# Performance work log

Hardware: AMD Instinct MI355X
Metric: run time of the kernel (lower is better)

## Reference

```python
import jax, jax.numpy as jnp
import numpy as np

N = 50000          # nodes
E = 800000         # edges (avg degree 16)
D = 128            # feature dim
MSG_EPS = 1e-7     # GENConv eps added to relu(msg)
SM_EPS = 1e-16     # pyg softmax denominator eps
BN_EPS = 1e-5
LN_EPS = 1e-5


def setup_inputs() -> dict:
    key = jax.random.key(0)
    ks = jax.random.split(key, 6)
    x = jax.random.normal(ks[0], (N, D), dtype=jnp.float32)
    edge_index = jax.random.randint(ks[1], (2, E), 0, N, dtype=jnp.int32)
    t = jnp.array(1.0, dtype=jnp.float32)
    W1 = jax.random.normal(ks[2], (D, 2 * D), dtype=jnp.float32) / np.sqrt(D).astype(np.float32)
    b1 = jnp.zeros((2 * D,), jnp.float32)
    bn_gamma = jnp.ones((2 * D,), jnp.float32)
    bn_beta = jnp.zeros((2 * D,), jnp.float32)
    W2 = jax.random.normal(ks[3], (2 * D, D), dtype=jnp.float32) / np.sqrt(2 * D).astype(np.float32)
    b2 = jnp.zeros((D,), jnp.float32)
    ln_gamma = jnp.ones((D,), jnp.float32)
    ln_beta = jnp.zeros((D,), jnp.float32)
    return {"x": x, "edge_index": edge_index, "t": t, "W1": W1, "b1": b1,
            "bn_gamma": bn_gamma, "bn_beta": bn_beta, "W2": W2, "b2": b2,
            "ln_gamma": ln_gamma, "ln_beta": ln_beta}


def reference(x, edge_index, t, W1, b1, bn_gamma, bn_beta, W2, b2, ln_gamma, ln_beta):
    src, dst = edge_index[0], edge_index[1]
    # --- GENConv message: relu(x_j) + eps  -> [E, D]
    msg = jax.nn.relu(x[src]) + MSG_EPS
    # --- softmax aggregation over incoming edges per dst node, per feature
    logits = t * msg                                            # [E, D]
    seg_max = jax.ops.segment_max(logits, dst, num_segments=N)  # [N, D]
    seg_max = jnp.where(jnp.isfinite(seg_max), seg_max, 0.0)    # empty segments -> 0
    ex = jnp.exp(logits - seg_max[dst])                         # [E, D]
    denom = jax.ops.segment_sum(ex, dst, num_segments=N)        # [N, D]
    alpha = ex / (denom[dst] + SM_EPS)                          # [E, D]
    agg = jax.ops.segment_sum(alpha * msg, dst, num_segments=N) # [N, D]
    # --- GENConv update: MLP(agg + x), MLP = Lin(D,2D)->BN->ReLU->Lin(2D,D)
    h = agg + x
    h = h @ W1 + b1                                             # [N, 2D]
    mu = jnp.mean(h, axis=0)
    var = jnp.var(h, axis=0)
    h = (h - mu) * jax.lax.rsqrt(var + BN_EPS) * bn_gamma + bn_beta
    h = jax.nn.relu(h)
    h = h @ W2 + b2                                             # [N, D]
    # --- LayerNorm -> ReLU -> (dropout p=0 noop) -> residual
    mu2 = jnp.mean(h, axis=-1, keepdims=True)
    var2 = jnp.mean(jnp.square(h - mu2), axis=-1, keepdims=True)
    h = (h - mu2) * jax.lax.rsqrt(var2 + LN_EPS) * ln_gamma + ln_beta
    h = jax.nn.relu(h)
    return x + h
```

## Files before the change

kernel.cpp:

```cpp
#include <hip/hip_runtime.h>

#define D 128
#define D2 256
#define BSH 5
#define BNODES 32
#define NBMAX 2048
#define CAP 640
#define PCHUNK 4096
#define REP 32
#define CSTRIDE 16
#define ZWORDS (2 * REP * 256 + NBMAX * CSTRIDE)

typedef __attribute__((ext_vector_type(8))) short short8;
typedef __attribute__((ext_vector_type(4))) float f32x4;

__device__ inline unsigned short f2b(float f) {
  unsigned u = __float_as_uint(f);
  unsigned r = (u + 0x7FFFu + ((u >> 16) & 1u)) >> 16;
  return (unsigned short)r;
}
__device__ inline float lo2f(unsigned u) { return __uint_as_float(u << 16); }
__device__ inline float hi2f(unsigned u) { return __uint_as_float(u & 0xffff0000u); }

__global__ __launch_bounds__(256) void prep_kernel(
    const float* __restrict__ x, const float* __restrict__ W1,
    const float* __restrict__ W2, const float* __restrict__ tptr,
    unsigned short* __restrict__ mb,
    unsigned short* __restrict__ W1f, unsigned short* __restrict__ W2f,
    float* __restrict__ zbase, int total4) {
  int idx = blockIdx.x * 256 + threadIdx.x;
  if (idx < 32768) {
    int k = idx >> 8, n = idx & 255;
    int t = n >> 4, m16 = n & 15;
    int kk = k >> 5, quad = (k >> 3) & 3, j = k & 7;
    W1f[(((t * 4 + kk) * 64 + quad * 16 + m16) << 3) + j] = f2b(W1[idx]);
  } else if (idx < 65536) {
    int i = idx - 32768;
    int k = i >> 7, n = i & 127;
    int t = n >> 4, m16 = n & 15;
    int kk = k >> 5, quad = (k >> 3) & 3, j = k & 7;
    W2f[(((t * 8 + kk) * 64 + quad * 16 + m16) << 3) + j] = f2b(W2[i]);
  } else if (idx < 65536 + total4) {
    int i = idx - 65536;
    float scl = tptr[0] * 1.4426950408889634f;
    float4 v = reinterpret_cast<const float4*>(x)[i];
    unsigned lo = (unsigned)f2b(scl * (fmaxf(v.x, 0.f) + 1e-7f)) |
                  ((unsigned)f2b(scl * (fmaxf(v.y, 0.f) + 1e-7f)) << 16);
    unsigned hi = (unsigned)f2b(scl * (fmaxf(v.z, 0.f) + 1e-7f)) |
                  ((unsigned)f2b(scl * (fmaxf(v.w, 0.f) + 1e-7f)) << 16);
    reinterpret_cast<uint2*>(mb)[i] = make_uint2(lo, hi);
  } else if (idx < 65536 + total4 + 32) {
    reinterpret_cast<uint2*>(mb)[idx - 65536] = make_uint2(0u, 0u);
  } else if (idx < 65536 + total4 + 32 + ZWORDS) {
    zbase[idx - (65536 + total4 + 32)] = 0.f;
  }
}

__global__ __launch_bounds__(256) void part_kernel(const int* __restrict__ ei,
                                                   int* __restrict__ cursor,
                                                   unsigned* __restrict__ pairbuf,
                                                   int E, int nb) {
  __shared__ int cnt[NBMAX];
  __shared__ int base[NBMAX];
  int tid = threadIdx.x;
  int c0 = blockIdx.x * PCHUNK;
  int nE = min(PCHUNK, E - c0);
  for (int i = tid; i < nb; i += 256) cnt[i] = 0;
  __syncthreads();
  for (int j = tid; j < nE; j += 256) {
    int dst = ei[E + c0 + j];
    atomicAdd(&cnt[dst >> BSH], 1);
  }
  __syncthreads();
  for (int i = tid; i < nb; i += 256) {
    int c = cnt[i];
    base[i] = (c > 0) ? atomicAdd(&cursor[i * CSTRIDE], c) : 0;
    cnt[i] = 0;
  }
  __syncthreads();
  for (int j = tid; j < nE; j += 256) {
    int e = c0 + j;
    int dst = ei[E + e];
    int src = ei[e];
    int b = dst >> BSH;
    int r = base[b] + atomicAdd(&cnt[b], 1);
    if (r < CAP)
      pairbuf[(size_t)b * CAP + r] =
          (unsigned)src | ((unsigned)(dst & (BNODES - 1)) << 16);
  }
}

__global__ __launch_bounds__(512) void agg2_kernel(const float* __restrict__ x,
                                                   const unsigned short* __restrict__ mb,
                                                   const unsigned* __restrict__ pairbuf,
                                                   const int* __restrict__ cursor,
                                                   const float* __restrict__ tptr,
                                                   unsigned short* __restrict__ h0b, int N) {
  __shared__ int soff[CAP + 4 * BNODES];
  __shared__ int cnt[BNODES], off[BNODES], run[BNODES], pcnt[BNODES];
  int b = blockIdx.x;
  int tid = threadIdx.x;
  int Eb = min(cursor[b * CSTRIDE], CAP);
  if (tid < BNODES) { cnt[tid] = 0; run[tid] = 0; }
  __syncthreads();
  for (int j = tid; j < Eb; j += 512)
    atomicAdd(&cnt[pairbuf[(size_t)b * CAP + j] >> 16], 1);
  __syncthreads();
  if (tid < BNODES) {
    int c = cnt[tid];
    int pc = (c + 3) & ~3;
    pcnt[tid] = pc;
    int s = pc;
#pragma unroll
    for (int st = 1; st < 32; st <<= 1) {
      int u = __shfl_up(s, st, 32);
      if ((tid & 31) >= st) s += u;
    }
    off[tid] = s - pc;
  }
  __syncthreads();
  for (int j = tid; j < Eb; j += 512) {
    unsigned p = pairbuf[(size_t)b * CAP + j];
    int dl = p >> 16;
    int r = atomicAdd(&run[dl], 1);
    soff[off[dl] + r] = (int)(p & 0xffffu) << 8;
  }
  if (tid < BNODES) {
    int o = off[tid];
    for (int r = cnt[tid]; r < pcnt[tid]; ++r) soff[o + r] = N << 8;
  }
  __syncthreads();

  int w = tid >> 6;
  int l = tid & 63;
  int half = l >> 5;
  int l32 = l & 31;
  float numscale = 0.69314718055994531f / tptr[0];
  int laneoff = l32 << 3;
  const char* mbase = (const char*)mb;

#define PROC(W)                                        \
  do {                                                 \
    float u0 = lo2f((W).x), u1 = hi2f((W).x);          \
    float u2 = lo2f((W).y), u3 = hi2f((W).y);          \
    float e0, e1, e2, e3;                              \
    asm("v_exp_f32 %0, %1" : "=v"(e0) : "v"(u0));      \
    asm("v_exp_f32 %0, %1" : "=v"(e1) : "v"(u1));      \
    asm("v_exp_f32 %0, %1" : "=v"(e2) : "v"(u2));      \
    asm("v_exp_f32 %0, %1" : "=v"(e3) : "v"(u3));      \
    den0 += e0; num0 = fmaf(e0, u0, num0);             \
    den1 += e1; num1 = fmaf(e1, u1, num1);             \
    den2 += e2; num2 = fmaf(e2, u2, num2);             \
    den3 += e3; num3 = fmaf(e3, u3, num3);             \
  } while (0)

#pragma unroll
  for (int p = 0; p < 2; ++p) {
    int ln = (p << 4) | (w << 1) | half;
    int n = (b << BSH) + ln;
    if (n >= N) continue;
    int s0 = off[ln];
    int dn = pcnt[ln];
    float den0 = 0.f, num0 = 0.f, den1 = 0.f, num1 = 0.f;
    float den2 = 0.f, num2 = 0.f, den3 = 0.f, num3 = 0.f;
    if (dn > 0) {
      uint2 uu[4];
#pragma unroll
      for (int q = 0; q < 4; ++q)
        uu[q] = *(const uint2*)(mbase + (soff[s0 + q] | laneoff));
      for (int j = 4; j < dn; j += 4) {
        uint2 vv[4];
#pragma unroll
        for (int q = 0; q < 4; ++q)
          vv[q] = *(const uint2*)(mbase + (soff[s0 + j + q] | laneoff));
#pragma unroll
        for (int q = 0; q < 4; ++q) PROC(uu[q]);
#pragma unroll
        for (int q = 0; q < 4; ++q) uu[q] = vv[q];
      }
#pragma unroll
      for (int q = 0; q < 4; ++q) PROC(uu[q]);
      float fnpad = (float)(dn - cnt[ln]);
      den0 -= fnpad; den1 -= fnpad; den2 -= fnpad; den3 -= fnpad;
    }
    size_t idx = ((size_t)n << 7) + (l32 << 2);
    float4 xv = *reinterpret_cast<const float4*>(x + idx);
    float v0 = num0 * numscale / (den0 + 1e-16f) + xv.x;
    float v1 = num1 * numscale / (den1 + 1e-16f) + xv.y;
    float v2 = num2 * numscale / (den2 + 1e-16f) + xv.z;
    float v3 = num3 * numscale / (den3 + 1e-16f) + xv.w;
    uint2 o;
    o.x = (unsigned)f2b(v0) | ((unsigned)f2b(v1) << 16);
    o.y = (unsigned)f2b(v2) | ((unsigned)f2b(v3) << 16);
    *reinterpret_cast<uint2*>(h0b + idx) = o;
  }
#undef PROC
}

__global__ __launch_bounds__(256) void gemm1_mfma(
    const unsigned short* __restrict__ h0b, const unsigned short* __restrict__ W1f,
    unsigned short* __restrict__ h1b,
    float* __restrict__ bnsum, float* __restrict__ bnsumsq, int M) {
  __shared__ unsigned short lt[4][64][72];
  int tid = threadIdx.x;
  int w = tid >> 6;
  int l = tid & 63;
  int m16 = l & 15;
  int quad = l >> 4;
  int r0 = blockIdx.x * 64;

  f32x4 acc[4][4];
#pragma unroll
  for (int rt = 0; rt < 4; ++rt)
#pragma unroll
    for (int ct = 0; ct < 4; ++ct) acc[rt][ct] = (f32x4){0.f, 0.f, 0.f, 0.f};

#pragma unroll
  for (int kk = 0; kk < 4; ++kk) {
    short8 bfr[4];
#pragma unroll
    for (int ct = 0; ct < 4; ++ct)
      bfr[ct] = *reinterpret_cast<const short8*>(
          W1f + ((((w * 4 + ct) * 4 + kk) * 64 + l) << 3));
    short8 a[4];
#pragma unroll
    for (int rt = 0; rt < 4; ++rt) {
      int row = min(r0 + rt * 16 + m16, M - 1);
      a[rt] = *reinterpret_cast<const short8*>(h0b + (size_t)row * D + kk * 32 + quad * 8);
    }
#pragma unroll
    for (int rt = 0; rt < 4; ++rt)
#pragma unroll
      for (int ct = 0; ct < 4; ++ct)
        acc[rt][ct] = __builtin_amdgcn_mfma_f32_16x16x32_bf16(a[rt], bfr[ct], acc[rt][ct], 0, 0, 0);
  }

  int rep = (blockIdx.x & (REP - 1)) << 8;
#pragma unroll
  for (int ct = 0; ct < 4; ++ct) {
    int col = w * 64 + ct * 16 + m16;
    float cs = 0.f, cq = 0.f;
#pragma unroll
    for (int rt = 0; rt < 4; ++rt) {
      int rloc = rt * 16 + quad * 4;
#pragma unroll
      for (int reg = 0; reg < 4; ++reg) {
        float val = acc[rt][ct][reg];
        if (r0 + rloc + reg < M) {
          cs += val;
          cq += val * val;
        }
        lt[w][rloc + reg][ct * 16 + m16] = f2b(val);
      }
    }
    cs += __shfl_xor(cs, 16, 64);
    cs += __shfl_xor(cs, 32, 64);
    cq += __shfl_xor(cq, 16, 64);
    cq += __shfl_xor(cq, 32, 64);
    if (quad == 0) {
      atomicAdd(&bnsum[rep + col], cs);
      atomicAdd(&bnsumsq[rep + col], cq);
    }
  }

  int row = r0 + l;
  if (row < M) {
    const unsigned short* src = &lt[w][l][0];
    unsigned short* dst = h1b + (size_t)row * D2 + w * 64;
#pragma unroll
    for (int j = 0; j < 8; ++j)
      *reinterpret_cast<short8*>(dst + j * 8) =
          *reinterpret_cast<const short8*>(src + j * 8);
  }
}

__global__ __launch_bounds__(256) void gemm2_mfma(
    const unsigned short* __restrict__ h1b, const unsigned short* __restrict__ W2f,
    const float* __restrict__ b2, const float* __restrict__ bnsum,
    const float* __restrict__ bnsumsq, const float* __restrict__ bng,
    const float* __restrict__ bnb, const float* __restrict__ lng,
    const float* __restrict__ lnb, const float* __restrict__ x,
    float* __restrict__ out, int M) {
  __shared__ float lnp[64][2], lnp2[64][2];
  __shared__ float sS[D2], sH[D2];
  int tid = threadIdx.x;
  {
    float s = 0.f, q = 0.f;
#pragma unroll
    for (int r = 0; r < REP; ++r) {
      s += bnsum[(r << 8) + tid];
      q += bnsumsq[(r << 8) + tid];
    }
    float invM = 1.f / (float)M;
    float mu = s * invM;
    float var = q * invM - mu * mu;
    float sc = bng[tid] * rsqrtf(var + 1e-5f);
    sS[tid] = sc;
    sH[tid] = bnb[tid] - mu * sc;
  }
  __syncthreads();

  int w = tid >> 6;
  int l = tid & 63;
  int m16 = l & 15;
  int quad = l >> 4;
  int rb = w >> 1, cb = w & 1;
  int r00 = blockIdx.x * 64;

  f32x4 acc[2][4];
#pragma unroll
  for (int rt = 0; rt < 2; ++rt)
#pragma unroll
    for (int ct = 0; ct < 4; ++ct) acc[rt][ct] = (f32x4){0.f, 0.f, 0.f, 0.f};

#pragma unroll
  for (int kk = 0; kk < 8; ++kk) {
    int base = kk * 32 + quad * 8;
    f32x4 s0 = *reinterpret_cast<const f32x4*>(&sS[base]);
    f32x4 s1 = *reinterpret_cast<const f32x4*>(&sS[base + 4]);
    f32x4 g0 = *reinterpret_cast<const f32x4*>(&sH[base]);
    f32x4 g1 = *reinterpret_cast<const f32x4*>(&sH[base + 4]);
    short8 a[2];
#pragma unroll
    for (int rt = 0; rt < 2; ++rt) {
      int row = min(r00 + rb * 32 + rt * 16 + m16, M - 1);
      uint4 raw = *reinterpret_cast<const uint4*>(h1b + (size_t)row * D2 + base);
      unsigned wds[4] = {raw.x, raw.y, raw.z, raw.w};
      unsigned ow[4];
#pragma unroll
      for (int q = 0; q < 4; ++q) {
        f32x4 sv = (q < 2) ? s0 : s1;
        f32x4 gv = (q < 2) ? g0 : g1;
        int e = (q & 1) * 2;
        float v0 = fmaxf(lo2f(wds[q]) * sv[e] + gv[e], 0.f);
        float v1 = fmaxf(hi2f(wds[q]) * sv[e + 1] + gv[e + 1], 0.f);
        ow[q] = (unsigned)f2b(v0) | ((unsigned)f2b(v1) << 16);
      }
      uint4 packed = make_uint4(ow[0], ow[1], ow[2], ow[3]);
      a[rt] = *reinterpret_cast<short8*>(&packed);
    }
    short8 bfr[4];
#pragma unroll
    for (int ct = 0; ct < 4; ++ct)
      bfr[ct] = *reinterpret_cast<const short8*>(
          W2f + ((((cb * 4 + ct) * 8 + kk) * 64 + l) << 3));
#pragma unroll
    for (int rt = 0; rt < 2; ++rt)
#pragma unroll
      for (int ct = 0; ct < 4; ++ct)
        acc[rt][ct] = __builtin_amdgcn_mfma_f32_16x16x32_bf16(a[rt], bfr[ct], acc[rt][ct], 0, 0, 0);
  }

  float b2v[4], lgv[4], lbv[4];
#pragma unroll
  for (int ct = 0; ct < 4; ++ct) {
    int col = cb * 64 + ct * 16 + m16;
    b2v[ct] = b2[col];
    lgv[ct] = lng[col];
    lbv[ct] = lnb[col];
  }

#pragma unroll
  for (int rt = 0; rt < 2; ++rt) {
#pragma unroll
    for (int reg = 0; reg < 4; ++reg) {
      float s = 0.f, s2 = 0.f;
#pragma unroll
      for (int ct = 0; ct < 4; ++ct) {
        float v = acc[rt][ct][reg] + b2v[ct];
        s += v;
        s2 += v * v;
      }
#pragma unroll
      for (int msk = 1; msk < 16; msk <<= 1) {
        s += __shfl_xor(s, msk, 64);
        s2 += __shfl_xor(s2, msk, 64);
      }
      if (m16 == 0) {
        int rl = rb * 32 + rt * 16 + quad * 4 + reg;
        lnp[rl][cb] = s;
        lnp2[rl][cb] = s2;
      }
    }
  }
  __syncthreads();

#pragma unroll
  for (int rt = 0; rt < 2; ++rt) {
#pragma unroll
    for (int reg = 0; reg < 4; ++reg) {
      int rl = rb * 32 + rt * 16 + quad * 4 + reg;
      int row = r00 + rl;
      float s = lnp[rl][0] + lnp[rl][1];
      float s2 = lnp2[rl][0] + lnp2[rl][1];
      float mu = s * (1.f / 128.f);
      float var = s2 * (1.f / 128.f) - mu * mu;
      float inv = rsqrtf(var + 1e-5f);
      if (row < M) {
#pragma unroll
        for (int ct = 0; ct < 4; ++ct) {
          int col = cb * 64 + ct * 16 + m16;
          float v = acc[rt][ct][reg] + b2v[ct];
          float h = fmaxf((v - mu) * inv * lgv[ct] + lbv[ct], 0.f);
          out[(size_t)row * D + col] = x[(size_t)row * D + col] + h;
        }
      }
    }
  }
}

extern "C" void kernel_launch(void* const* d_in, const int* in_sizes, int n_in,
                              void* d_out, int out_size, void* d_ws, size_t ws_size,
                              hipStream_t stream) {
  const float* x   = (const float*)d_in[0];
  const int*   ei  = (const int*)d_in[1];
  const float* t   = (const float*)d_in[2];
  const float* W1  = (const float*)d_in[3];
  const float* bng = (const float*)d_in[5];
  const float* bnb = (const float*)d_in[6];
  const float* W2  = (const float*)d_in[7];
  const float* b2  = (const float*)d_in[8];
  const float* lng = (const float*)d_in[9];
  const float* lnb = (const float*)d_in[10];
  float* out = (float*)d_out;

  int N = in_sizes[0] / D;
  int E = in_sizes[1] / 2;
  size_t nd = (size_t)N * D;
  int nb = (N + BNODES - 1) >> BSH;

  unsigned short* mb  = (unsigned short*)d_ws;
  unsigned short* h0b = mb + nd + 128;
  unsigned short* h1b = h0b + nd;
  unsigned short* W1f = h1b + 2 * nd;
  unsigned short* W2f = W1f + 32768;
  float* bnsum   = (float*)(W2f + 32768);
  float* bnsumsq = bnsum + REP * 256;
  int* cursor    = (int*)(bnsumsq + REP * 256);
  unsigned* pairbuf = (unsigned*)(cursor + NBMAX * CSTRIDE);

  int total4 = (int)(nd / 4);
  int ptotal = 65536 + total4 + 32 + ZWORDS;
  prep_kernel<<<(ptotal + 255) / 256, 256, 0, stream>>>(x, W1, W2, t, mb, W1f, W2f,
                                                        bnsum, total4);

  part_kernel<<<(E + PCHUNK - 1) / PCHUNK, 256, 0, stream>>>(ei, cursor, pairbuf, E, nb);
  agg2_kernel<<<nb, 512, 0, stream>>>(x, mb, pairbuf, cursor, t, h0b, N);

  gemm1_mfma<<<(N + 63) / 64, 256, 0, stream>>>(h0b, W1f, h1b, bnsum, bnsumsq, N);
  gemm2_mfma<<<(N + 63) / 64, 256, 0, stream>>>(h1b, W2f, b2, bnsum, bnsumsq,
                                                bng, bnb, lng, lnb, x, out, N);
}
```

Measured before the change: 205.7 us.

## Recompute GEMM1 inside GEMM2 instead of storing the bf16 hidden activation

The first GEMM kernel now only accumulates BatchNorm statistics and no longer writes the N x 2D bf16 intermediate. The second kernel recomputes h0 @ W1 per tile, applies BN and ReLU, stages the result in shared memory, and feeds it to the W2 GEMM. This removes the global write and re-read of the 2D-wide intermediate (about 25 MB each way) at the cost of doing GEMM1 twice and using more LDS per block in the fused kernel.

```diff
diff --git a/kernel.cpp b/kernel.cpp
--- a/kernel.cpp
+++ b/kernel.cpp
@@ -197,11 +197,9 @@
 #undef PROC
 }
 
-__global__ __launch_bounds__(256) void gemm1_mfma(
+__global__ __launch_bounds__(256) void gemm1_stats(
     const unsigned short* __restrict__ h0b, const unsigned short* __restrict__ W1f,
-    unsigned short* __restrict__ h1b,
     float* __restrict__ bnsum, float* __restrict__ bnsumsq, int M) {
-  __shared__ unsigned short lt[4][64][72];
   int tid = threadIdx.x;
   int w = tid >> 6;
   int l = tid & 63;
@@ -250,7 +248,6 @@
           cs += val;
           cq += val * val;
         }
-        lt[w][rloc + reg][ct * 16 + m16] = f2b(val);
       }
     }
     cs += __shfl_xor(cs, 16, 64);
@@ -262,25 +259,16 @@
       atomicAdd(&bnsumsq[rep + col], cq);
     }
   }
-
-  int row = r0 + l;
-  if (row < M) {
-    const unsigned short* src = &lt[w][l][0];
-    unsigned short* dst = h1b + (size_t)row * D2 + w * 64;
-#pragma unroll
-    for (int j = 0; j < 8; ++j)
-      *reinterpret_cast<short8*>(dst + j * 8) =
-          *reinterpret_cast<const short8*>(src + j * 8);
-  }
 }
 
 __global__ __launch_bounds__(256) void gemm2_mfma(
-    const unsigned short* __restrict__ h1b, const unsigned short* __restrict__ W2f,
-    const float* __restrict__ b2, const float* __restrict__ bnsum,
-    const float* __restrict__ bnsumsq, const float* __restrict__ bng,
-    const float* __restrict__ bnb, const float* __restrict__ lng,
-    const float* __restrict__ lnb, const float* __restrict__ x,
-    float* __restrict__ out, int M) {
+    const unsigned short* __restrict__ h0b, const unsigned short* __restrict__ W1f,
+    const unsigned short* __restrict__ W2f, const float* __restrict__ b2,
+    const float* __restrict__ bnsum, const float* __restrict__ bnsumsq,
+    const float* __restrict__ bng, const float* __restrict__ bnb,
+    const float* __restrict__ lng, const float* __restrict__ lnb,
+    const float* __restrict__ x, float* __restrict__ out, int M) {
+  __shared__ unsigned short lt[4][64][72];
   __shared__ float lnp[64][2], lnp2[64][2];
   __shared__ float sS[D2], sH[D2];
   int tid = threadIdx.x;
@@ -304,9 +292,54 @@
   int l = tid & 63;
   int m16 = l & 15;
   int quad = l >> 4;
+  int r0 = blockIdx.x * 64;
+
+  {
+    f32x4 acc[4][4];
+#pragma unroll
+    for (int rt = 0; rt < 4; ++rt)
+#pragma unroll
+      for (int ct = 0; ct < 4; ++ct) acc[rt][ct] = (f32x4){0.f, 0.f, 0.f, 0.f};
+
+#pragma unroll
+    for (int kk = 0; kk < 4; ++kk) {
+      short8 bfr[4];
+#pragma unroll
+      for (int ct = 0; ct < 4; ++ct)
+        bfr[ct] = *reinterpret_cast<const short8*>(
+            W1f + ((((w * 4 + ct) * 4 + kk) * 64 + l) << 3));
+      short8 a[4];
+#pragma unroll
+      for (int rt = 0; rt < 4; ++rt) {
+        int row = min(r0 + rt * 16 + m16, M - 1);
+        a[rt] = *reinterpret_cast<const short8*>(h0b + (size_t)row * D + kk * 32 + quad * 8);
+      }
+#pragma unroll
+      for (int rt = 0; rt < 4; ++rt)
+#pragma unroll
+        for (int ct = 0; ct < 4; ++ct)
+          acc[rt][ct] = __builtin_amdgcn_mfma_f32_16x16x32_bf16(a[rt], bfr[ct], acc[rt][ct], 0, 0, 0);
+    }
+
+#pragma unroll
+    for (int ct = 0; ct < 4; ++ct) {
+      int col = w * 64 + ct * 16 + m16;
+      float sc = sS[col];
+      float sh = sH[col];
+#pragma unroll
+      for (int rt = 0; rt < 4; ++rt) {
+        int rloc = rt * 16 + quad * 4;
+#pragma unroll
+        for (int reg = 0; reg < 4; ++reg) {
+          float h = fmaxf(acc[rt][ct][reg] * sc + sh, 0.f);
+          lt[w][rloc + reg][ct * 16 + m16] = f2b(h);
+        }
+      }
+    }
+  }
+  __syncthreads();
+
   int rb = w >> 1, cb = w & 1;
-  int r00 = blockIdx.x * 64;
-
   f32x4 acc[2][4];
 #pragma unroll
   for (int rt = 0; rt < 2; ++rt)
@@ -316,28 +349,11 @@
 #pragma unroll
   for (int kk = 0; kk < 8; ++kk) {
     int base = kk * 32 + quad * 8;
-    f32x4 s0 = *reinterpret_cast<const f32x4*>(&sS[base]);
-    f32x4 s1 = *reinterpret_cast<const f32x4*>(&sS[base + 4]);
-    f32x4 g0 = *reinterpret_cast<const f32x4*>(&sH[base]);
-    f32x4 g1 = *reinterpret_cast<const f32x4*>(&sH[base + 4]);
     short8 a[2];
 #pragma unroll
     for (int rt = 0; rt < 2; ++rt) {
-      int row = min(r00 + rb * 32 + rt * 16 + m16, M - 1);
-      uint4 raw = *reinterpret_cast<const uint4*>(h1b + (size_t)row * D2 + base);
-      unsigned wds[4] = {raw.x, raw.y, raw.z, raw.w};
-      unsigned ow[4];
-#pragma unroll
-      for (int q = 0; q < 4; ++q) {
-        f32x4 sv = (q < 2) ? s0 : s1;
-        f32x4 gv = (q < 2) ? g0 : g1;
-        int e = (q & 1) * 2;
-        float v0 = fmaxf(lo2f(wds[q]) * sv[e] + gv[e], 0.f);
-        float v1 = fmaxf(hi2f(wds[q]) * sv[e + 1] + gv[e + 1], 0.f);
-        ow[q] = (unsigned)f2b(v0) | ((unsigned)f2b(v1) << 16);
-      }
-      uint4 packed = make_uint4(ow[0], ow[1], ow[2], ow[3]);
-      a[rt] = *reinterpret_cast<short8*>(&packed);
+      int rl = rb * 32 + rt * 16 + m16;
+      a[rt] = *reinterpret_cast<const short8*>(&lt[base >> 6][rl][base & 63]);
     }
     short8 bfr[4];
 #pragma unroll
@@ -390,7 +406,7 @@
 #pragma unroll
     for (int reg = 0; reg < 4; ++reg) {
       int rl = rb * 32 + rt * 16 + quad * 4 + reg;
-      int row = r00 + rl;
+      int row = r0 + rl;
       float s = lnp[rl][0] + lnp[rl][1];
       float s2 = lnp2[rl][0] + lnp2[rl][1];
       float mu = s * (1.f / 128.f);
@@ -431,8 +447,7 @@
 
   unsigned short* mb  = (unsigned short*)d_ws;
   unsigned short* h0b = mb + nd + 128;
-  unsigned short* h1b = h0b + nd;
-  unsigned short* W1f = h1b + 2 * nd;
+  unsigned short* W1f = h0b + nd;
   unsigned short* W2f = W1f + 32768;
   float* bnsum   = (float*)(W2f + 32768);
   float* bnsumsq = bnsum + REP * 256;
@@ -447,7 +462,7 @@
   part_kernel<<<(E + PCHUNK - 1) / PCHUNK, 256, 0, stream>>>(ei, cursor, pairbuf, E, nb);
   agg2_kernel<<<nb, 512, 0, stream>>>(x, mb, pairbuf, cursor, t, h0b, N);
 
-  gemm1_mfma<<<(N + 63) / 64, 256, 0, stream>>>(h0b, W1f, h1b, bnsum, bnsumsq, N);
-  gemm2_mfma<<<(N + 63) / 64, 256, 0, stream>>>(h1b, W2f, b2, bnsum, bnsumsq,
+  gemm1_stats<<<(N + 63) / 64, 256, 0, stream>>>(h0b, W1f, bnsum, bnsumsq, N);
+  gemm2_mfma<<<(N + 63) / 64, 256, 0, stream>>>(h0b, W1f, W2f, b2, bnsum, bnsumsq,
                                                 bng, bnb, lng, lnb, x, out, N);
 }
```

Result: no change. 205.8 us (+0.0%).
